# Performance work log

Hardware: AMD Instinct MI355X
Metric: run time of the kernel (lower is better)

The kernel has to match this reference:

```python
import jax, jax.numpy as jnp
import numpy as np
import math

B, T, N, D = 4, 12, 1024, 64
LN_EPS = 1e-5


def setup_inputs() -> dict:
    key = jax.random.key(0)
    k1, k2, k3 = jax.random.split(key, 3)
    X = jax.random.normal(k1, (B, T, N, D), dtype=jnp.float32)
    A = jax.random.uniform(k2, (N, N), dtype=jnp.float32)
    W = jax.random.normal(k3, (D, D), dtype=jnp.float32) * (1.0 / math.sqrt(D))
    gamma = jnp.ones((D,), dtype=jnp.float32)
    beta = jnp.zeros((D,), dtype=jnp.float32)
    return {"X": X, "A": A, "W": W, "gamma": gamma, "beta": beta}


def reference(X, A, W, gamma, beta):
    d = X.shape[-1]
    # dynamic attention scores: (b,t,n,m)
    scores = jnp.einsum('btnd,btmd->btnm', X, X)
    St = jax.nn.softmax(scores, axis=-1) / jnp.sqrt(jnp.float32(d)) + 1e-8
    # adjacency-gated dynamic graph: A (n,m) broadcast over (b,t)
    Ag = A[None, None, :, :] * St
    # graph conv: aggregate then linear (nn.Linear: H @ W.T), relu
    H = jnp.einsum('btnm,btmd->btnd', Ag, X)
    out = jax.nn.relu(H @ W.T)
    # layernorm over last dim
    mu = jnp.mean(out, axis=-1, keepdims=True)
    var = jnp.var(out, axis=-1, keepdims=True)
    out = (out - mu) * jax.lax.rsqrt(var + LN_EPS) * gamma + beta
    # residual
    return out + X
```

## Files before the change

kernel.cpp:

```cpp
#include <hip/hip_runtime.h>
#include <hip/hip_bf16.h>
#include <math.h>


typedef short bf16x8 __attribute__((ext_vector_type(8)));
typedef float f32x4  __attribute__((ext_vector_type(4)));
typedef float f32x16 __attribute__((ext_vector_type(16)));
typedef int   i32x4  __attribute__((ext_vector_type(4)));

constexpr int kN = 1024;
constexpr int kD = 64;
constexpr size_t kPlane    = 48u * 1024u * 64u;
constexpr size_t kAfShorts = 16u * 32u * 2048u;

#define MFMA32(a,b,c) __builtin_amdgcn_mfma_f32_32x32x16_bf16((a),(b),(c),0,0,0)
#define MFMA16(a,b,c) __builtin_amdgcn_mfma_f32_16x16x32_bf16((a),(b),(c),0,0,0)

__device__ __forceinline__ void splitv(float v, short& h, short& l) {
  unsigned u = __float_as_uint(v);
  h = (short)(u >> 16);
  float hf = __uint_as_float(u & 0xFFFF0000u);
  l = (short)(__float_as_uint(v - hf) >> 16);
}

__device__ __forceinline__ unsigned pkbf(float a, float b) {
  return (__float_as_uint(a) >> 16) | (__float_as_uint(b) & 0xFFFF0000u);
}

__global__ __launch_bounds__(256)
void presplit(const float* __restrict__ X, short* __restrict__ Xh,
              short* __restrict__ Xl, short* __restrict__ XTh)
{
  __shared__ short Sh[64][68], Sl[64][68];
  const int t  = threadIdx.x;
  const int bt = blockIdx.x >> 4;
  const int mb = blockIdx.x & 15;
  const size_t base = (size_t)bt * 65536 + (size_t)mb * 64 * 64;

#pragma unroll
  for (int k = 0; k < 4; ++k) {
    int idx = t + k * 256;
    int row = idx >> 4;
    int c4  = (idx & 15) * 4;
    float4 v = *(const float4*)(X + base + row * 64 + c4);
    short h0,l0,h1,l1,h2,l2,h3,l3;
    splitv(v.x, h0, l0); splitv(v.y, h1, l1);
    splitv(v.z, h2, l2); splitv(v.w, h3, l3);
    short4 hv = make_short4(h0, h1, h2, h3);
    short4 lv = make_short4(l0, l1, l2, l3);
    *(short4*)(Xh + base + row * 64 + c4) = hv;
    *(short4*)(Xl + base + row * 64 + c4) = lv;
    *(short4*)&Sh[row][c4] = hv;
    *(short4*)&Sl[row][c4] = lv;
  }
  __syncthreads();

  const size_t tbase = (size_t)bt * 65536 + (size_t)mb * 64;
#pragma unroll
  for (int k = 0; k < 2; ++k) {
    int idx = t + k * 256;
    int d   = idx >> 3;
    int m8  = (idx & 7) * 8;
    bf16x8 hv;
#pragma unroll
    for (int j = 0; j < 8; ++j) hv[j] = Sh[m8 + j][d];
    *(bf16x8*)(XTh + tbase + (size_t)d * 1024 + m8) = hv;
  }
}

__global__ __launch_bounds__(256)
void prearr_Abf(const float* __restrict__ A, short* __restrict__ Af)
{
  const int qt  = blockIdx.x >> 5;
  const int gks = blockIdx.x & 31;
  const int kb  = gks * 32;
  const int s   = threadIdx.x;
  short* dst = Af + ((size_t)(qt * 32 + gks) * 2048);

  const int qw = s >> 7;
  const int ln = (s >> 1) & 63;
  const int p  = s & 1;
  const int q  = qt * 64 + qw * 32 + (ln & 31);
  const int h  = ln >> 5;
  const int k0 = kb + 16 * p + 4 * h;
  float4 f0 = *(const float4*)(A + (size_t)q * kN + k0);
  float4 f1 = *(const float4*)(A + (size_t)q * kN + k0 + 8);
  i32x4 u;
  u[0] = (int)pkbf(f0.x, f0.y); u[1] = (int)pkbf(f0.z, f0.w);
  u[2] = (int)pkbf(f1.x, f1.y); u[3] = (int)pkbf(f1.z, f1.w);
  *(i32x4*)(dst + (size_t)qw * 1024 + ln * 16 + p * 8) = u;
}

template<int AMODE>
__global__ __launch_bounds__(256)
void sdgcn_v9(const float* __restrict__ X, const float* __restrict__ A,
              const float* __restrict__ W, const float* __restrict__ gamma,
              const float* __restrict__ beta, float* __restrict__ out,
              const short* __restrict__ Xh, const short* __restrict__ Xl,
              const short* __restrict__ XTh, const short* __restrict__ Af)
{
  __shared__ __align__(16) unsigned char LB[28672];

  const int t    = threadIdx.x;
  const int wave = t >> 6;
  const int lane = t & 63;
  const int kg   = wave >> 1;
  const int qw   = wave & 1;
  const int half = lane >> 5;
  const int l31  = lane & 31;
  const int bid  = blockIdx.x;
  const int swz  = (bid & 7) * 96 + (bid >> 3);
  const int bt   = swz >> 4;
  const int qt   = swz & 15;
  const int qblk = qt * 64;
  const size_t xb = (size_t)bt * 65536;

  short* Khg  = (short*)(LB + kg * 9216);
  short* Klg  = Khg + 2304;
  short* Vthg = (short*)(LB + 18432 + kg * 5120);
  float* aM   = (float*)LB;
  float* aZ   = aM + 128;
  float* aF   = aZ + 128;
  float* Har  = (float*)(LB + 1792);

  const int qmine = qblk + qw * 32 + l31;
  bf16x8 qh[4], qlo[4];
#pragma unroll
  for (int c = 0; c < 4; ++c) {
    const size_t off = xb + (size_t)qmine * kD + 16 * c + half * 8;
    qh[c]  = *(const bf16x8*)(Xh + off);
    qlo[c] = *(const bf16x8*)(Xl + off);
  }

  f32x16 o0, o1;
#pragma unroll
  for (int r = 0; r < 16; ++r) { o0[r] = 0.f; o1[r] = 0.f; }
  float mrun = -INFINITY, Z = 0.f;

  const int tg = t & 127;

  auto ldK = [&](int kb, int j, bf16x8& h, bf16x8& l) {
    int ck = tg + 128 * j; int kr = ck >> 3; int kc = (ck & 7) * 8;
    size_t off = xb + (size_t)(kb + kr) * kD + kc;
    h = *(const bf16x8*)(Xh + off);
    l = *(const bf16x8*)(Xl + off);
  };
  auto ldV = [&](int kb, int j, bf16x8& h) {
    int cv = tg + 128 * j; int vd = cv >> 2; int vm = (cv & 3) * 8;
    h = *(const bf16x8*)(XTh + xb + (size_t)vd * 1024 + kb + vm);
  };
  auto stK = [&](int j, bf16x8 h, bf16x8 l) {
    int ck = tg + 128 * j; int kr = ck >> 3; int kc = (ck & 7) * 8;
    *(bf16x8*)&Khg[kr * 72 + kc] = h;
    *(bf16x8*)&Klg[kr * 72 + kc] = l;
  };
  auto stV = [&](int j, bf16x8 h) {
    int cv = tg + 128 * j; int vd = cv >> 2; int vm = (cv & 3) * 8;
    *(bf16x8*)&Vthg[vd * 40 + vm] = h;
  };

  {
    bf16x8 a0,a1,b0,b1,c0,d0;
    ldK(kg * 512, 0, a0, a1); ldK(kg * 512, 1, b0, b1);
    ldV(kg * 512, 0, c0);     ldV(kg * 512, 1, d0);
    stK(0, a0, a1); stK(1, b0, b1); stV(0, c0); stV(1, d0);
  }
  i32x4 aA = {0,0,0,0}, aB = {0,0,0,0};
  if (AMODE == 1) {
    const short* Ab = Af + ((size_t)(qt * 32 + kg * 16) * 2048)
                         + (size_t)qw * 1024 + (lane << 4);
    aA = *(const i32x4*)(Ab);
    aB = *(const i32x4*)(Ab + 8);
  }
  __syncthreads();

  for (int ks = 0; ks < 16; ++ks) {
    const int kb = kg * 512 + ks * 32;
    const bool pfm = (ks + 1) < 16;

    bf16x8 nk0h,nk0l,nk1h,nk1l,nv0,nv1;
    if (pfm) {
      ldK(kb + 32, 0, nk0h, nk0l); ldK(kb + 32, 1, nk1h, nk1l);
      ldV(kb + 32, 0, nv0);        ldV(kb + 32, 1, nv1);
    }
    i32x4 naA = {0,0,0,0}, naB = {0,0,0,0};
    if (AMODE == 1 && pfm) {
      const short* Ab = Af + ((size_t)(qt * 32 + kg * 16 + ks + 1) * 2048)
                           + (size_t)qw * 1024 + (lane << 4);
      naA = *(const i32x4*)(Ab);
      naB = *(const i32x4*)(Ab + 8);
    }

    float agv[16];
    if (AMODE == 1) {
      unsigned u[8] = {(unsigned)aA[0],(unsigned)aA[1],(unsigned)aA[2],(unsigned)aA[3],
                       (unsigned)aB[0],(unsigned)aB[1],(unsigned)aB[2],(unsigned)aB[3]};
#pragma unroll
      for (int m = 0; m < 8; ++m) {
        agv[2*m]   = __uint_as_float(u[m] << 16);
        agv[2*m+1] = __uint_as_float(u[m] & 0xFFFF0000u);
      }
    } else {
      const float* Arow = A + (size_t)qmine * kN + kb + 4 * half;
      float4 ag0 = *(const float4*)(Arow);
      float4 ag1 = *(const float4*)(Arow + 8);
      float4 ag2 = *(const float4*)(Arow + 16);
      float4 ag3 = *(const float4*)(Arow + 24);
#pragma unroll
      for (int e = 0; e < 4; ++e) {
        agv[e] = ag0[e]; agv[4+e] = ag1[e]; agv[8+e] = ag2[e]; agv[12+e] = ag3[e];
      }
    }

    f32x16 sa;
#pragma unroll
    for (int r = 0; r < 16; ++r) sa[r] = 0.f;
    __builtin_amdgcn_s_setprio(1);
#pragma unroll
    for (int c = 0; c < 4; ++c) {
      bf16x8 kh = *(const bf16x8*)&Khg[l31 * 72 + 16 * c + half * 8];
      bf16x8 kl = *(const bf16x8*)&Klg[l31 * 72 + 16 * c + half * 8];
      sa = MFMA32(kh, qh[c],  sa);
      sa = MFMA32(kh, qlo[c], sa);
      sa = MFMA32(kl, qh[c],  sa);
    }
    __builtin_amdgcn_s_setprio(0);

    float sm = sa[0];
#pragma unroll
    for (int r = 1; r < 16; ++r) sm = fmaxf(sm, sa[r]);
    sm = fmaxf(sm, __shfl_xor(sm, 32, 64));
    if (__any(sm > mrun + 8.f)) {
      const float nm = fmaxf(mrun, sm);
      const float f  = __expf(mrun - nm);
      mrun = nm; Z *= f;
#pragma unroll
      for (int r = 0; r < 16; ++r) {
        const float fr = __shfl(f, (r & 3) + 8 * (r >> 2) + 4 * half, 64);
        o0[r] *= fr; o1[r] *= fr;
      }
    }
    float zt = 0.f;
    float pa[16];
#pragma unroll
    for (int r = 0; r < 16; ++r) {
      const float pv = __expf(sa[r] - mrun);
      zt += pv;
      pa[r] = pv * agv[r];
    }
    zt += __shfl_xor(zt, 32, 64);
    Z += zt;

    unsigned du[8], su[8];
#pragma unroll
    for (int j = 0; j < 8; ++j) du[j] = pkbf(pa[2*j], pa[2*j+1]);
#pragma unroll
    for (int j = 0; j < 8; ++j) su[j] = (unsigned)__shfl_xor((int)du[j], 32, 64);
    const bool lo = (half == 0);
    i32x4 w0, w1;
    w0[0] = lo ? du[0] : su[2]; w0[1] = lo ? du[1] : su[3];
    w0[2] = lo ? su[0] : du[2]; w0[3] = lo ? su[1] : du[3];
    w1[0] = lo ? du[4] : su[6]; w1[1] = lo ? du[5] : su[7];
    w1[2] = lo ? su[4] : du[6]; w1[3] = lo ? su[5] : du[7];
    bf16x8 pf0 = *(bf16x8*)&w0;
    bf16x8 pf1 = *(bf16x8*)&w1;

    {
      bf16x8 v0 = *(const bf16x8*)&Vthg[l31 * 40 + half * 8];
      bf16x8 v1 = *(const bf16x8*)&Vthg[l31 * 40 + 16 + half * 8];
      bf16x8 v2 = *(const bf16x8*)&Vthg[(32 + l31) * 40 + half * 8];
      bf16x8 v3 = *(const bf16x8*)&Vthg[(32 + l31) * 40 + 16 + half * 8];
      __builtin_amdgcn_s_setprio(1);
      o0 = MFMA32(pf0, v0, o0);
      o0 = MFMA32(pf1, v1, o0);
      o1 = MFMA32(pf0, v2, o1);
      o1 = MFMA32(pf1, v3, o1);
      __builtin_amdgcn_s_setprio(0);
    }

    __syncthreads();
    if (pfm) {
      stK(0, nk0h, nk0l); stK(1, nk1h, nk1l);
      stV(0, nv0);        stV(1, nv1);
    }
    __syncthreads();
    aA = naA; aB = naB;
  }

  if (lane < 32) {
    aM[kg * 64 + qw * 32 + l31] = mrun;
    aZ[kg * 64 + qw * 32 + l31] = Z;
  }
  if (kg == 1) {
#pragma unroll
    for (int r = 0; r < 16; ++r) {
      const int qq = qw * 32 + (r & 3) + 8 * (r >> 2) + 4 * half;
      Har[qq * 68 + l31]      = o0[r];
      Har[qq * 68 + l31 + 32] = o1[r];
    }
  }
  __syncthreads();
  if (kg == 1 && lane < 32) {
    const int q = qw * 32 + l31;
    const float ma = aM[q], mb = mrun;
    const float m  = fmaxf(ma, mb);
    const float fa = __expf(ma - m), fb = __expf(mb - m);
    const float Zs = aZ[q] * fa + Z * fb;
    aF[q]       = fa;
    aF[64 + q]  = fb;
    aF[128 + q] = 1.0f / (8.0f * Zs);
  }
  __syncthreads();
  if (kg == 0) {
#pragma unroll
    for (int r = 0; r < 16; ++r) {
      const int qq = qw * 32 + (r & 3) + 8 * (r >> 2) + 4 * half;
      const float fa = aF[qq], fb = aF[64 + qq];
      Har[qq * 68 + l31]      = o0[r] * fa + Har[qq * 68 + l31]      * fb;
      Har[qq * 68 + l31 + 32] = o1[r] * fa + Har[qq * 68 + l31 + 32] * fb;
    }
  }
  __syncthreads();

  const int g  = lane >> 4;
  const int ql = lane & 15;
  const int er = wave * 16;
  const float i8z = aF[128 + er + ql];

  bf16x8 hh[2], hl[2];
#pragma unroll
  for (int kk = 0; kk < 2; ++kk) {
    const float* hp = &Har[(er + ql) * 68 + kk * 32 + g * 8];
    float4 v0 = *(const float4*)hp;
    float4 v1 = *(const float4*)(hp + 4);
    float v[8] = {v0.x*i8z, v0.y*i8z, v0.z*i8z, v0.w*i8z,
                  v1.x*i8z, v1.y*i8z, v1.z*i8z, v1.w*i8z};
#pragma unroll
    for (int e = 0; e < 8; ++e) { short a, b; splitv(v[e], a, b); hh[kk][e] = a; hl[kk][e] = b; }
  }

  f32x4 lin[4];
#pragma unroll
  for (int c = 0; c < 4; ++c) {
    bf16x8 wh[2], wl[2];
#pragma unroll
    for (int kk = 0; kk < 2; ++kk) {
      const float* wp = W + (size_t)(c * 16 + ql) * kD + kk * 32 + g * 8;
      float4 v0 = *(const float4*)wp;
      float4 v1 = *(const float4*)(wp + 4);
      float v[8] = {v0.x, v0.y, v0.z, v0.w, v1.x, v1.y, v1.z, v1.w};
#pragma unroll
      for (int e = 0; e < 8; ++e) { short a, b; splitv(v[e], a, b); wh[kk][e] = a; wl[kk][e] = b; }
    }
    f32x4 acc = {0.f, 0.f, 0.f, 0.f};
    acc = MFMA16(hh[0], wh[0], acc);
    acc = MFMA16(hh[1], wh[1], acc);
    acc = MFMA16(hh[0], wl[0], acc);
    acc = MFMA16(hh[1], wl[1], acc);
    acc = MFMA16(hl[0], wh[0], acc);
    acc = MFMA16(hl[1], wh[1], acc);
    lin[c] = acc;
  }

  float rl[4][4];
#pragma unroll
  for (int c = 0; c < 4; ++c)
#pragma unroll
    for (int r = 0; r < 4; ++r) rl[c][r] = fmaxf(lin[c][r], 0.f);

  float mu[4], rstd[4];
#pragma unroll
  for (int r = 0; r < 4; ++r) {
    float s1 = rl[0][r] + rl[1][r] + rl[2][r] + rl[3][r];
    float s2 = rl[0][r]*rl[0][r] + rl[1][r]*rl[1][r] + rl[2][r]*rl[2][r] + rl[3][r]*rl[3][r];
#pragma unroll
    for (int off = 1; off < 16; off <<= 1) {
      s1 += __shfl_xor(s1, off, 64);
      s2 += __shfl_xor(s2, off, 64);
    }
    mu[r] = s1 * (1.f / 64.f);
    const float var = s2 * (1.f / 64.f) - mu[r] * mu[r];
    rstd[r] = rsqrtf(var + 1e-5f);
  }

#pragma unroll
  for (int c = 0; c < 4; ++c) {
    const float gm = gamma[c * 16 + ql];
    const float bb = beta[c * 16 + ql];
#pragma unroll
    for (int r = 0; r < 4; ++r) {
      const int qrow = qblk + er + 4 * g + r;
      const size_t off = ((size_t)bt * kN + qrow) * kD + c * 16 + ql;
      out[off] = (rl[c][r] - mu[r]) * rstd[r] * gm + bb + X[off];
    }
  }
}

extern "C" void kernel_launch(void* const* d_in, const int* in_sizes, int n_in,
                              void* d_out, int out_size, void* d_ws, size_t ws_size,
                              hipStream_t stream) {
  const float* X     = (const float*)d_in[0];
  const float* A     = (const float*)d_in[1];
  const float* W     = (const float*)d_in[2];
  const float* gamma = (const float*)d_in[3];
  const float* beta  = (const float*)d_in[4];
  float* out = (float*)d_out;

  short* Xh  = (short*)d_ws;
  short* Xl  = Xh  + kPlane;
  short* XTh = Xl  + kPlane;
  short* Af  = XTh + kPlane;

  const size_t need = (3 * kPlane + kAfShorts) * sizeof(short);

  presplit<<<dim3(48 * 16), 256, 0, stream>>>(X, Xh, Xl, XTh);
  if (ws_size >= need) {
    prearr_Abf<<<dim3(16 * 32), 256, 0, stream>>>(A, Af);
    sdgcn_v9<1><<<dim3(48 * 16), 256, 0, stream>>>(X, A, W, gamma, beta, out,
                                                   Xh, Xl, XTh, Af);
  } else {
    sdgcn_v9<0><<<dim3(48 * 16), 256, 0, stream>>>(X, A, W, gamma, beta, out,
                                                   Xh, Xl, XTh, Af);
  }
}
```

Before: 71.64 us.

## Double-buffer K/V shared tiles with XOR swizzle, one barrier per step

Shared memory now holds two buffers of the K-hi, K-lo and V-transpose tiles, and the key loop is unrolled by two. The next tile is written into the spare buffer while the current one is being computed, so each step needs one barrier instead of two. The padded row strides (72 and 40) are replaced by unpadded rows with an XOR swizzle to avoid bank conflicts. LDS per block grows from 28 KB to 48 KB, which may lower the number of resident blocks per CU.

```diff
diff --git a/kernel.cpp b/kernel.cpp
--- a/kernel.cpp
+++ b/kernel.cpp
@@ -93,13 +93,13 @@
 
 template<int AMODE>
 __global__ __launch_bounds__(256)
-void sdgcn_v9(const float* __restrict__ X, const float* __restrict__ A,
-              const float* __restrict__ W, const float* __restrict__ gamma,
-              const float* __restrict__ beta, float* __restrict__ out,
-              const short* __restrict__ Xh, const short* __restrict__ Xl,
-              const short* __restrict__ XTh, const short* __restrict__ Af)
+void sdgcn_v12(const float* __restrict__ X, const float* __restrict__ A,
+               const float* __restrict__ W, const float* __restrict__ gamma,
+               const float* __restrict__ beta, float* __restrict__ out,
+               const short* __restrict__ Xh, const short* __restrict__ Xl,
+               const short* __restrict__ XTh, const short* __restrict__ Af)
 {
-  __shared__ __align__(16) unsigned char LB[28672];
+  __shared__ __align__(16) unsigned char LB[49152];
 
   const int t    = threadIdx.x;
   const int wave = t >> 6;
@@ -115,13 +115,16 @@
   const int qblk = qt * 64;
   const size_t xb = (size_t)bt * 65536;
 
-  short* Khg  = (short*)(LB + kg * 9216);
-  short* Klg  = Khg + 2304;
-  short* Vthg = (short*)(LB + 18432 + kg * 5120);
-  float* aM   = (float*)LB;
-  float* aZ   = aM + 128;
-  float* aF   = aZ + 128;
-  float* Har  = (float*)(LB + 1792);
+  short* Kh0 = (short*)(LB + kg * 12288);
+  short* Kl0 = Kh0 + 2048;
+  short* Vt0 = Kh0 + 4096;
+  short* Kh1 = (short*)(LB + 24576 + kg * 12288);
+  short* Kl1 = Kh1 + 2048;
+  short* Vt1 = Kh1 + 4096;
+  float* aM  = (float*)LB;
+  float* aZ  = aM + 128;
+  float* aF  = aZ + 128;
+  float* Har = (float*)(LB + 1792);
 
   const int qmine = qblk + qw * 32 + l31;
   bf16x8 qh[4], qlo[4];
@@ -149,42 +152,26 @@
     int cv = tg + 128 * j; int vd = cv >> 2; int vm = (cv & 3) * 8;
     h = *(const bf16x8*)(XTh + xb + (size_t)vd * 1024 + kb + vm);
   };
-  auto stK = [&](int j, bf16x8 h, bf16x8 l) {
-    int ck = tg + 128 * j; int kr = ck >> 3; int kc = (ck & 7) * 8;
-    *(bf16x8*)&Khg[kr * 72 + kc] = h;
-    *(bf16x8*)&Klg[kr * 72 + kc] = l;
+  auto stK = [&](short* Kh, short* Kl, int j, bf16x8 h, bf16x8 l) {
+    int ck = tg + 128 * j; int kr = ck >> 3; int u = ck & 7;
+    int off = kr * 64 + ((u ^ (kr & 7)) << 3);
+    *(bf16x8*)&Kh[off] = h;
+    *(bf16x8*)&Kl[off] = l;
   };
-  auto stV = [&](int j, bf16x8 h) {
-    int cv = tg + 128 * j; int vd = cv >> 2; int vm = (cv & 3) * 8;
-    *(bf16x8*)&Vthg[vd * 40 + vm] = h;
+  auto stV = [&](short* Vt, int j, bf16x8 h) {
+    int cv = tg + 128 * j; int vd = cv >> 2; int u = cv & 3;
+    int off = vd * 32 + ((u ^ (vd & 3)) << 3);
+    *(bf16x8*)&Vt[off] = h;
   };
 
-  {
-    bf16x8 a0,a1,b0,b1,c0,d0;
-    ldK(kg * 512, 0, a0, a1); ldK(kg * 512, 1, b0, b1);
-    ldV(kg * 512, 0, c0);     ldV(kg * 512, 1, d0);
-    stK(0, a0, a1); stK(1, b0, b1); stV(0, c0); stV(1, d0);
-  }
   i32x4 aA = {0,0,0,0}, aB = {0,0,0,0};
-  if (AMODE == 1) {
-    const short* Ab = Af + ((size_t)(qt * 32 + kg * 16) * 2048)
-                         + (size_t)qw * 1024 + (lane << 4);
-    aA = *(const i32x4*)(Ab);
-    aB = *(const i32x4*)(Ab + 8);
-  }
-  __syncthreads();
-
-  for (int ks = 0; ks < 16; ++ks) {
+
+  auto compute = [&](int ks, const short* Khg, const short* Klg,
+                     const short* Vtg, bool pfA) {
     const int kb = kg * 512 + ks * 32;
-    const bool pfm = (ks + 1) < 16;
-
-    bf16x8 nk0h,nk0l,nk1h,nk1l,nv0,nv1;
-    if (pfm) {
-      ldK(kb + 32, 0, nk0h, nk0l); ldK(kb + 32, 1, nk1h, nk1l);
-      ldV(kb + 32, 0, nv0);        ldV(kb + 32, 1, nv1);
-    }
+
     i32x4 naA = {0,0,0,0}, naB = {0,0,0,0};
-    if (AMODE == 1 && pfm) {
+    if (AMODE == 1 && pfA) {
       const short* Ab = Af + ((size_t)(qt * 32 + kg * 16 + ks + 1) * 2048)
                            + (size_t)qw * 1024 + (lane << 4);
       naA = *(const i32x4*)(Ab);
@@ -218,8 +205,9 @@
     __builtin_amdgcn_s_setprio(1);
 #pragma unroll
     for (int c = 0; c < 4; ++c) {
-      bf16x8 kh = *(const bf16x8*)&Khg[l31 * 72 + 16 * c + half * 8];
-      bf16x8 kl = *(const bf16x8*)&Klg[l31 * 72 + 16 * c + half * 8];
+      const int off = l31 * 64 + (((2 * c + half) ^ (l31 & 7)) << 3);
+      bf16x8 kh = *(const bf16x8*)&Khg[off];
+      bf16x8 kl = *(const bf16x8*)&Klg[off];
       sa = MFMA32(kh, qh[c],  sa);
       sa = MFMA32(kh, qlo[c], sa);
       sa = MFMA32(kl, qh[c],  sa);
@@ -266,10 +254,11 @@
     bf16x8 pf1 = *(bf16x8*)&w1;
 
     {
-      bf16x8 v0 = *(const bf16x8*)&Vthg[l31 * 40 + half * 8];
-      bf16x8 v1 = *(const bf16x8*)&Vthg[l31 * 40 + 16 + half * 8];
-      bf16x8 v2 = *(const bf16x8*)&Vthg[(32 + l31) * 40 + half * 8];
-      bf16x8 v3 = *(const bf16x8*)&Vthg[(32 + l31) * 40 + 16 + half * 8];
+      const int dxa = l31 & 3;
+      bf16x8 v0 = *(const bf16x8*)&Vtg[l31 * 32 + ((half ^ dxa) << 3)];
+      bf16x8 v1 = *(const bf16x8*)&Vtg[l31 * 32 + (((2 + half) ^ dxa) << 3)];
+      bf16x8 v2 = *(const bf16x8*)&Vtg[(32 + l31) * 32 + ((half ^ dxa) << 3)];
+      bf16x8 v3 = *(const bf16x8*)&Vtg[(32 + l31) * 32 + (((2 + half) ^ dxa) << 3)];
       __builtin_amdgcn_s_setprio(1);
       o0 = MFMA32(pf0, v0, o0);
       o0 = MFMA32(pf1, v1, o0);
@@ -277,14 +266,48 @@
       o1 = MFMA32(pf1, v3, o1);
       __builtin_amdgcn_s_setprio(0);
     }
-
+    aA = naA; aB = naB;
+  };
+
+  {
+    bf16x8 a0,a1,b0,b1,c0,d0;
+    ldK(kg * 512, 0, a0, a1); ldK(kg * 512, 1, b0, b1);
+    ldV(kg * 512, 0, c0);     ldV(kg * 512, 1, d0);
+    stK(Kh0, Kl0, 0, a0, a1); stK(Kh0, Kl0, 1, b0, b1);
+    stV(Vt0, 0, c0);          stV(Vt0, 1, d0);
+  }
+  if (AMODE == 1) {
+    const short* Ab = Af + ((size_t)(qt * 32 + kg * 16) * 2048)
+                         + (size_t)qw * 1024 + (lane << 4);
+    aA = *(const i32x4*)(Ab);
+    aB = *(const i32x4*)(Ab + 8);
+  }
+  __syncthreads();
+
+  for (int ks = 0; ks < 16; ks += 2) {
+    bf16x8 k0h,k0l,k1h,k1l,vr0,vr1;
+    ldK(kg * 512 + (ks + 1) * 32, 0, k0h, k0l);
+    ldK(kg * 512 + (ks + 1) * 32, 1, k1h, k1l);
+    ldV(kg * 512 + (ks + 1) * 32, 0, vr0);
+    ldV(kg * 512 + (ks + 1) * 32, 1, vr1);
+    compute(ks, Kh0, Kl0, Vt0, true);
+    stK(Kh1, Kl1, 0, k0h, k0l); stK(Kh1, Kl1, 1, k1h, k1l);
+    stV(Vt1, 0, vr0);           stV(Vt1, 1, vr1);
     __syncthreads();
-    if (pfm) {
-      stK(0, nk0h, nk0l); stK(1, nk1h, nk1l);
-      stV(0, nv0);        stV(1, nv1);
+
+    const bool more = (ks + 2) < 16;
+    if (more) {
+      ldK(kg * 512 + (ks + 2) * 32, 0, k0h, k0l);
+      ldK(kg * 512 + (ks + 2) * 32, 1, k1h, k1l);
+      ldV(kg * 512 + (ks + 2) * 32, 0, vr0);
+      ldV(kg * 512 + (ks + 2) * 32, 1, vr1);
+    }
+    compute(ks + 1, Kh1, Kl1, Vt1, more);
+    if (more) {
+      stK(Kh0, Kl0, 0, k0h, k0l); stK(Kh0, Kl0, 1, k1h, k1l);
+      stV(Vt0, 0, vr0);           stV(Vt0, 1, vr1);
     }
     __syncthreads();
-    aA = naA; aB = naB;
   }
 
   if (lane < 32) {
@@ -416,10 +439,10 @@
   presplit<<<dim3(48 * 16), 256, 0, stream>>>(X, Xh, Xl, XTh);
   if (ws_size >= need) {
     prearr_Abf<<<dim3(16 * 32), 256, 0, stream>>>(A, Af);
-    sdgcn_v9<1><<<dim3(48 * 16), 256, 0, stream>>>(X, A, W, gamma, beta, out,
-                                                   Xh, Xl, XTh, Af);
+    sdgcn_v12<1><<<dim3(48 * 16), 256, 0, stream>>>(X, A, W, gamma, beta, out,
+                                                    Xh, Xl, XTh, Af);
   } else {
-    sdgcn_v9<0><<<dim3(48 * 16), 256, 0, stream>>>(X, A, W, gamma, beta, out,
-                                                   Xh, Xl, XTh, Af);
-  }
-}
+    sdgcn_v12<0><<<dim3(48 * 16), 256, 0, stream>>>(X, A, W, gamma, beta, out,
+                                                    Xh, Xl, XTh, Af);
+  }
+}
```

New measurement: 72.70 us. No clear change (+1.5%).
